# Performance work log

Measured on AMD Instinct MI355X. Metric: run time of the kernel, lower is better.

Reference implementation:

```python
import jax, jax.numpy as jnp
import numpy as np

B, F, S, D, H = 32, 4096, 8, 512, 2048
N_ITERS = 3
EPS = 1e-8
SCALE = D ** -0.5
LN_EPS = 1e-5  # torch LayerNorm default


def setup_inputs() -> dict:
    key = jax.random.key(0)
    ks = jax.random.split(key, 16)
    w = lambda k, shp: (jax.random.normal(k, shp) * 0.02).astype(jnp.float32)
    d = {
        "slots": jax.random.normal(ks[0], (B, S, D), dtype=jnp.float32),
        "features": jax.random.normal(ks[1], (B, F, D), dtype=jnp.float32),
        # projection weights, stored (in, out) so y = x @ W
        "w_k": w(ks[2], (D, D)),
        "w_v": w(ks[3], (D, D)),
        "w_q": w(ks[4], (D, D)),
        # layer norms
        "ln_feat_w": jnp.ones(D, jnp.float32), "ln_feat_b": jnp.zeros(D, jnp.float32),
        "ln_slot_w": jnp.ones(D, jnp.float32), "ln_slot_b": jnp.zeros(D, jnp.float32),
        # GRUCell (torch layout: gates [r, z, n] stacked on dim0 of [3D, D])
        "gru_w_ih": w(ks[5], (3 * D, D)),
        "gru_w_hh": w(ks[6], (3 * D, D)),
        "gru_b_ih": jnp.zeros(3 * D, jnp.float32),
        "gru_b_hh": jnp.zeros(3 * D, jnp.float32),
        # residual MLP: LN -> Linear(D,H) -> relu -> Linear(H,D)
        "ln_mlp_w": jnp.ones(D, jnp.float32), "ln_mlp_b": jnp.zeros(D, jnp.float32),
        "mlp_w1": w(ks[7], (D, H)), "mlp_b1": jnp.zeros(H, jnp.float32),
        "mlp_w2": w(ks[8], (H, D)), "mlp_b2": jnp.zeros(D, jnp.float32),
    }
    return d


def _ln(x, w, b):
    m = jnp.mean(x, axis=-1, keepdims=True)
    v = jnp.mean(jnp.square(x - m), axis=-1, keepdims=True)
    return (x - m) * jax.lax.rsqrt(v + LN_EPS) * w + b


def _gru_cell(x, h, w_ih, w_hh, b_ih, b_hh):
    # torch.nn.GRUCell semantics; x,h: [..., D]
    gi = x @ w_ih.T + b_ih
    gh = h @ w_hh.T + b_hh
    i_r, i_z, i_n = jnp.split(gi, 3, axis=-1)
    h_r, h_z, h_n = jnp.split(gh, 3, axis=-1)
    r = jax.nn.sigmoid(i_r + h_r)
    z = jax.nn.sigmoid(i_z + h_z)
    n = jnp.tanh(i_n + r * h_n)
    return (1.0 - z) * n + z * h


def reference(slots, features, w_k, w_v, w_q, ln_feat_w, ln_feat_b,
              ln_slot_w, ln_slot_b, gru_w_ih, gru_w_hh, gru_b_ih, gru_b_hh,
              ln_mlp_w, ln_mlp_b, mlp_w1, mlp_b1, mlp_w2, mlp_b2):
    f = _ln(features, ln_feat_w, ln_feat_b)          # [B,F,D]
    keys = f @ w_k                                    # [B,F,D]
    values = f @ w_v                                  # [B,F,D]
    pre_norm_attn = None
    for _ in range(N_ITERS):
        s_n = _ln(slots, ln_slot_w, ln_slot_b)        # [B,S,D]
        q = s_n @ w_q                                 # [B,S,D]
        dots = jnp.einsum('bsd,bfd->bsf', q, keys) * SCALE
        pre_norm_attn = jax.nn.softmax(dots, axis=1)  # softmax over SLOTS
        attn = pre_norm_attn + EPS
        attn = attn / jnp.sum(attn, axis=-1, keepdims=True)
        updates = jnp.einsum('bsf,bfd->bsd', attn, values)
        slots = _gru_cell(updates, s_n, gru_w_ih, gru_w_hh, gru_b_ih, gru_b_hh)
        # residual MLP with initial LayerNorm
        h = _ln(slots, ln_mlp_w, ln_mlp_b)
        h = jax.nn.relu(h @ mlp_w1 + mlp_b1) @ mlp_w2 + mlp_b2
        slots = slots + h
    return slots, pre_norm_attn
```

## Files before the change

kernel.cpp:

```cpp
#include <hip/hip_runtime.h>
#include <hip/hip_bf16.h>
#include <stdint.h>

typedef __hip_bfloat16 bf16;
typedef unsigned short ushort_t;

#define B_ 32
#define F_ 4096
#define S_ 8
#define D_ 512
#define H_ 2048
#define LN_EPS 1e-5f
#define EPS_ 1e-8f
#define SCALE_ 0.044194173824159216f

__device__ __forceinline__ float b2f(ushort_t u){
  union { uint32_t i; float f; } c; c.i = ((uint32_t)u) << 16; return c.f;
}
__device__ __forceinline__ float4 ld4f(const float* p){ return *(const float4*)p; }
__device__ __forceinline__ float4 ld4h(const ushort_t* p){
  ushort4 u = *(const ushort4*)p;
  return make_float4(b2f(u.x), b2f(u.y), b2f(u.z), b2f(u.w));
}
__device__ __forceinline__ float allsum64(float v){
  #pragma unroll
  for (int o = 1; o < 64; o <<= 1) v += __shfl_xor(v, o, 64);
  return v;
}
__device__ __forceinline__ float blockSum256(float v, float* sh){
  v = allsum64(v);
  int wid = threadIdx.x >> 6, lane = threadIdx.x & 63;
  __syncthreads();
  if (lane == 0) sh[wid] = v;
  __syncthreads();
  return sh[0] + sh[1] + sh[2] + sh[3];
}
__device__ __forceinline__ float dynld(const void* p, int i, bool f32){
  return f32 ? ((const float*)p)[i] : b2f(((const ushort_t*)p)[i]);
}

__global__ void detect_dtype(const uint32_t* __restrict__ w, int* __restrict__ flag){
  __shared__ int sh;
  if (threadIdx.x == 0) sh = 0;
  __syncthreads();
  int c = 0;
  for (int i = threadIdx.x; i < 4096; i += 256){
    uint32_t e = (w[i] >> 7) & 0xFF;
    if (e == 0 || e >= 0xBF) c++;
  }
  atomicAdd(&sh, c);
  __syncthreads();
  if (threadIdx.x == 0) *flag = (sh >= 100) ? 1 : 0;
}

template<int TRANS_B, int A_DYN, int B_DYN, int A_CMB>
__global__ __launch_bounds__(256) void gemm64(
    const void* __restrict__ A, const void* __restrict__ B,
    const void* __restrict__ Abias, float* __restrict__ C,
    int M, int N, int K, int kLen, size_t aPart, const int* __restrict__ flag)
{
  const bool f32 = (*flag != 0);
  const bool aF = A_DYN ? f32 : true;
  const bool bF = B_DYN ? f32 : true;
  __shared__ float As[16][68];
  __shared__ float Bs[16][68];
  const int tid = threadIdx.x;
  const int m0 = blockIdx.x * 64, n0 = blockIdx.y * 64;
  const int kBeg = blockIdx.z * kLen;
  const int tm = (tid & 15) * 4, tn = (tid >> 4) * 4;
  const int ar = tid >> 2;
  const int ac = (tid & 3) * 4;
  const int br = tid >> 4;
  const int bc = (tid & 15) * 4;
  float acc[4][4] = {};

  for (int kc = kBeg; kc < kBeg + kLen; kc += 16){
    size_t aidx = (size_t)(m0 + ar) * K + kc + ac;
    float4 a4;
    if (A_CMB){
      const float* Af = (const float*)A;
      float4 s0 = ld4f(Af + aidx);
      float4 s1 = ld4f(Af + aPart + aidx);
      float4 s2 = ld4f(Af + 2 * aPart + aidx);
      float4 s3 = ld4f(Af + 3 * aPart + aidx);
      float bx0 = dynld(Abias, kc + ac + 0, f32);
      float bx1 = dynld(Abias, kc + ac + 1, f32);
      float bx2 = dynld(Abias, kc + ac + 2, f32);
      float bx3 = dynld(Abias, kc + ac + 3, f32);
      a4.x = fmaxf(s0.x + s1.x + s2.x + s3.x + bx0, 0.0f);
      a4.y = fmaxf(s0.y + s1.y + s2.y + s3.y + bx1, 0.0f);
      a4.z = fmaxf(s0.z + s1.z + s2.z + s3.z + bx2, 0.0f);
      a4.w = fmaxf(s0.w + s1.w + s2.w + s3.w + bx3, 0.0f);
    } else {
      a4 = aF ? ld4f((const float*)A + aidx) : ld4h((const ushort_t*)A + aidx);
    }
    As[ac+0][ar] = a4.x; As[ac+1][ar] = a4.y; As[ac+2][ar] = a4.z; As[ac+3][ar] = a4.w;
    if (!TRANS_B){
      size_t bidx = (size_t)(kc + br) * N + n0 + bc;
      float4 b4 = bF ? ld4f((const float*)B + bidx) : ld4h((const ushort_t*)B + bidx);
      Bs[br][bc+0] = b4.x; Bs[br][bc+1] = b4.y; Bs[br][bc+2] = b4.z; Bs[br][bc+3] = b4.w;
    } else {
      size_t bidx = (size_t)(n0 + ar) * K + kc + ac;
      float4 b4 = bF ? ld4f((const float*)B + bidx) : ld4h((const ushort_t*)B + bidx);
      Bs[ac+0][ar] = b4.x; Bs[ac+1][ar] = b4.y; Bs[ac+2][ar] = b4.z; Bs[ac+3][ar] = b4.w;
    }
    __syncthreads();
    #pragma unroll
    for (int k = 0; k < 16; k++){
      float av[4], bv[4];
      #pragma unroll
      for (int i = 0; i < 4; i++) av[i] = As[k][tm + i];
      #pragma unroll
      for (int j = 0; j < 4; j++) bv[j] = Bs[k][tn + j];
      #pragma unroll
      for (int i = 0; i < 4; i++)
        #pragma unroll
        for (int j = 0; j < 4; j++) acc[i][j] += av[i] * bv[j];
    }
    __syncthreads();
  }
  #pragma unroll
  for (int i = 0; i < 4; i++)
    #pragma unroll
    for (int j = 0; j < 4; j++)
      C[((size_t)blockIdx.z * M + m0 + tm + i) * N + n0 + tn + j] = acc[i][j];
}

__global__ __launch_bounds__(256) void combine4(
    const float* __restrict__ in, float* __restrict__ out, int sz)
{
  int i = blockIdx.x * 256 + threadIdx.x;
  out[i] = in[i] + in[sz + i] + in[2 * sz + i] + in[3 * sz + i];
}

__global__ __launch_bounds__(256) void gemm_gigh(
    const float* __restrict__ Ud, const float* __restrict__ Wvih,
    const float* __restrict__ s_n, const void* __restrict__ w_hh,
    float* __restrict__ gip, float* __restrict__ ghp,
    const int* __restrict__ flag)
{
  const bool f32 = (*flag != 0);
  const bool doGh = blockIdx.z >= 4;
  const int kz = blockIdx.z & 3;
  __shared__ float As[16][68];
  __shared__ float Bs[16][68];
  const int tid = threadIdx.x;
  const int m0 = blockIdx.x * 64, n0 = blockIdx.y * 64;
  const int kBeg = kz * 128;
  const int tm = (tid & 15) * 4, tn = (tid >> 4) * 4;
  const int ar = tid >> 2;
  const int ac = (tid & 3) * 4;
  const int br = tid >> 4;
  const int bc = (tid & 15) * 4;
  const float* A = doGh ? s_n : Ud;
  float acc[4][4] = {};

  for (int kc = kBeg; kc < kBeg + 128; kc += 16){
    float4 a4 = ld4f(A + (size_t)(m0 + ar) * 512 + kc + ac);
    As[ac+0][ar] = a4.x; As[ac+1][ar] = a4.y; As[ac+2][ar] = a4.z; As[ac+3][ar] = a4.w;
    if (!doGh){
      float4 b4 = ld4f(Wvih + (size_t)(kc + br) * 1536 + n0 + bc);
      Bs[br][bc+0] = b4.x; Bs[br][bc+1] = b4.y; Bs[br][bc+2] = b4.z; Bs[br][bc+3] = b4.w;
    } else {
      size_t bidx = (size_t)(n0 + ar) * 512 + kc + ac;
      float4 b4 = f32 ? ld4f((const float*)w_hh + bidx)
                      : ld4h((const ushort_t*)w_hh + bidx);
      Bs[ac+0][ar] = b4.x; Bs[ac+1][ar] = b4.y; Bs[ac+2][ar] = b4.z; Bs[ac+3][ar] = b4.w;
    }
    __syncthreads();
    #pragma unroll
    for (int k = 0; k < 16; k++){
      float av[4], bv[4];
      #pragma unroll
      for (int i = 0; i < 4; i++) av[i] = As[k][tm + i];
      #pragma unroll
      for (int j = 0; j < 4; j++) bv[j] = Bs[k][tn + j];
      #pragma unroll
      for (int i = 0; i < 4; i++)
        #pragma unroll
        for (int j = 0; j < 4; j++) acc[i][j] += av[i] * bv[j];
    }
    __syncthreads();
  }
  float* C = (doGh ? ghp : gip) + (size_t)kz * 256 * 1536;
  #pragma unroll
  for (int i = 0; i < 4; i++)
    #pragma unroll
    for (int j = 0; j < 4; j++)
      C[(size_t)(m0 + tm + i) * 1536 + n0 + tn + j] = acc[i][j];
}

__global__ __launch_bounds__(256, 2) void big_pass(
    const void* __restrict__ features, const float* __restrict__ qkp,
    const void* __restrict__ lnw, const void* __restrict__ lnb,
    void* __restrict__ d_out_base, float* __restrict__ Upart,
    float* __restrict__ Rpart, const int* __restrict__ flag)
{
  const bool F32 = (*flag != 0);
  __shared__ float Ubuf[4][S_ * D_];
  __shared__ float Rbuf[4][S_];
  __shared__ float pbuf[S_][256];
  const int b = blockIdx.y;
  const int tid = threadIdx.x;
  const int wid = tid >> 6, lane = tid & 63;
  const int fblock = blockIdx.x * 256;
  const int f0 = fblock + wid * 64;

  float lw[8], lb[8];
  #pragma unroll
  for (int j = 0; j < 8; j++){
    int d = 8 * lane + j;
    lw[j] = dynld(lnw, d, F32);
    lb[j] = dynld(lnb, d, F32);
  }
  float qkr[8][8];
  #pragma unroll
  for (int s = 0; s < 8; s++){
    const float* qp = qkp + (size_t)(b * S_ + s) * D_ + 8 * lane;
    float4 q0 = ld4f(qp);
    float4 q1 = ld4f(qp + 4);
    #pragma unroll
    for (int p = 1; p < 4; p++){
      const float* qq = qp + (size_t)p * 131072;
      float4 t0 = ld4f(qq), t1 = ld4f(qq + 4);
      q0.x += t0.x; q0.y += t0.y; q0.z += t0.z; q0.w += t0.w;
      q1.x += t1.x; q1.y += t1.y; q1.z += t1.z; q1.w += t1.w;
    }
    qkr[s][0]=q0.x; qkr[s][1]=q0.y; qkr[s][2]=q0.z; qkr[s][3]=q0.w;
    qkr[s][4]=q1.x; qkr[s][5]=q1.y; qkr[s][6]=q1.z; qkr[s][7]=q1.w;
  }
  float U[8][8];
  #pragma unroll
  for (int s = 0; s < 8; s++)
    #pragma unroll
    for (int j = 0; j < 8; j++) U[s][j] = 0.0f;
  float racc[8] = {0,0,0,0,0,0,0,0};

  const size_t base = ((size_t)b * F_ + f0) * D_ + 8 * lane;
  const float* fbf = (const float*)features + base;
  const ushort_t* fbh = (const ushort_t*)features + base;
  float4 nf0 = {}, nf1 = {}; uint4 nh = {};
  if (F32){ nf0 = *(const float4*)fbf; nf1 = *(const float4*)(fbf + 4); }
  else    { nh  = *(const uint4*)fbh; }

  for (int r = 0; r < 64; r++){
    float x[8];
    if (F32){
      float4 c0 = nf0, c1 = nf1;
      if (r < 63){
        nf0 = *(const float4*)(fbf + (size_t)(r + 1) * D_);
        nf1 = *(const float4*)(fbf + (size_t)(r + 1) * D_ + 4);
      }
      x[0]=c0.x; x[1]=c0.y; x[2]=c0.z; x[3]=c0.w;
      x[4]=c1.x; x[5]=c1.y; x[6]=c1.z; x[7]=c1.w;
    } else {
      uint4 cx = nh;
      if (r < 63) nh = *(const uint4*)(fbh + (size_t)(r + 1) * D_);
      x[0]=b2f(cx.x & 0xffff); x[1]=b2f(cx.x >> 16);
      x[2]=b2f(cx.y & 0xffff); x[3]=b2f(cx.y >> 16);
      x[4]=b2f(cx.z & 0xffff); x[5]=b2f(cx.z >> 16);
      x[6]=b2f(cx.w & 0xffff); x[7]=b2f(cx.w >> 16);
    }
    float sum = 0.0f;
    #pragma unroll
    for (int j = 0; j < 8; j++) sum += x[j];
    float mean = allsum64(sum) * (1.0f / 512.0f);
    float var = 0.0f;
    #pragma unroll
    for (int j = 0; j < 8; j++){ x[j] -= mean; var += x[j] * x[j]; }
    var = allsum64(var) * (1.0f / 512.0f);
    float rstd = 1.0f / sqrtf(var + LN_EPS);
    float y[8];
    #pragma unroll
    for (int j = 0; j < 8; j++) y[j] = x[j] * rstd * lw[j] + lb[j];

    float dt[8];
    #pragma unroll
    for (int s = 0; s < 8; s++){
      float t = 0.0f;
      #pragma unroll
      for (int j = 0; j < 8; j++) t += qkr[s][j] * y[j];
      dt[s] = allsum64(t) * SCALE_;
    }
    float mx = dt[0];
    #pragma unroll
    for (int s = 1; s < 8; s++) mx = fmaxf(mx, dt[s]);
    float p[8]; float den = 0.0f;
    #pragma unroll
    for (int s = 0; s < 8; s++){ p[s] = __expf(dt[s] - mx); den += p[s]; }
    float inv = 1.0f / den;
    #pragma unroll
    for (int s = 0; s < 8; s++) p[s] *= inv;
    #pragma unroll
    for (int s = 0; s < 8; s++) if (lane == s) pbuf[s][wid * 64 + r] = p[s];
    #pragma unroll
    for (int s = 0; s < 8; s++){
      float pe = p[s] + EPS_;
      racc[s] += pe;
      #pragma unroll
      for (int j = 0; j < 8; j++) U[s][j] += pe * y[j];
    }
  }
  #pragma unroll
  for (int s = 0; s < 8; s++){
    float* ub = &Ubuf[wid][s * D_ + 8 * lane];
    *(float4*)ub     = make_float4(U[s][0], U[s][1], U[s][2], U[s][3]);
    *(float4*)(ub+4) = make_float4(U[s][4], U[s][5], U[s][6], U[s][7]);
  }
  #pragma unroll
  for (int s = 0; s < 8; s++) if (lane == s) Rbuf[wid][s] = racc[s];
  __syncthreads();
  float* up = Upart + (size_t)(b * 16 + blockIdx.x) * S_ * D_;
  for (int e = tid; e < S_ * D_; e += 256)
    up[e] = Ubuf[0][e] + Ubuf[1][e] + Ubuf[2][e] + Ubuf[3][e];
  if (tid < 8)
    Rpart[(b * 16 + blockIdx.x) * S_ + tid] =
        Rbuf[0][tid] + Rbuf[1][tid] + Rbuf[2][tid] + Rbuf[3][tid];
  #pragma unroll
  for (int s = 0; s < 8; s++){
    size_t oi = 131072 + ((size_t)(b * S_ + s)) * F_ + fblock + tid;
    float pv = pbuf[s][tid];
    if (F32) ((float*)d_out_base)[oi] = pv;
    else     ((bf16*)d_out_base)[oi] = __float2bfloat16(pv);
  }
}

__global__ __launch_bounds__(256) void reduce_updates(
    const float* __restrict__ Upart, const float* __restrict__ Rpart,
    float* __restrict__ Ud)
{
  __shared__ float rinv;
  int bs = blockIdx.x;
  int b = bs >> 3, s = bs & 7;
  int t = threadIdx.x;
  if (t == 0){
    float r = 0.0f;
    for (int w = 0; w < 16; w++) r += Rpart[(b * 16 + w) * S_ + s];
    rinv = 1.0f / r;
  }
  __syncthreads();
  const float* up = Upart + ((size_t)(b * 16) * S_ + s) * D_;
  float ri = rinv;
  #pragma unroll
  for (int u = 0; u < 2; u++){
    int e = t + u * 256;
    float acc = 0.0f;
    for (int w = 0; w < 16; w++) acc += up[(size_t)w * S_ * D_ + e];
    Ud[((size_t)(b * S_ + s)) * D_ + e] = acc * ri;
  }
}

__global__ __launch_bounds__(256) void ln_rows(
    const float* __restrict__ x, const void* __restrict__ w,
    const void* __restrict__ b, float* __restrict__ y, const int* __restrict__ flag)
{
  const bool f32 = (*flag != 0);
  __shared__ float sh[4];
  int row = blockIdx.x, t = threadIdx.x;
  const float* xr = x + (size_t)row * D_;
  float v0 = xr[t], v1 = xr[t + 256];
  float mean = blockSum256(v0 + v1, sh) * (1.0f / 512.0f);
  float d0 = v0 - mean, d1 = v1 - mean;
  float var = blockSum256(d0 * d0 + d1 * d1, sh) * (1.0f / 512.0f);
  float rstd = 1.0f / sqrtf(var + LN_EPS);
  float w0 = dynld(w, t, f32),       w1 = dynld(w, t + 256, f32);
  float b0 = dynld(b, t, f32),       b1 = dynld(b, t + 256, f32);
  y[(size_t)row * D_ + t]       = d0 * rstd * w0 + b0;
  y[(size_t)row * D_ + t + 256] = d1 * rstd * w1 + b1;
}

__global__ __launch_bounds__(256) void gru_combine(
    const float* __restrict__ gip, const float* __restrict__ ghp,
    const void* __restrict__ b_ih, const void* __restrict__ b_hh,
    const float* __restrict__ sn, const void* __restrict__ lw,
    const void* __restrict__ lb, float* __restrict__ snew,
    float* __restrict__ lnm, const int* __restrict__ flag)
{
  const bool f32 = (*flag != 0);
  __shared__ float sh[4];
  int row = blockIdx.x, t = threadIdx.x;
  const float* snr = sn + (size_t)row * D_;
  float v[2];
  #pragma unroll
  for (int u = 0; u < 2; u++){
    int d = t + u * 256;
    float ir = 0, iz = 0, in_ = 0, hr = 0, hz = 0, hn = 0;
    #pragma unroll
    for (int p = 0; p < 4; p++){
      const float* gp = gip + (size_t)p * 393216 + (size_t)row * 1536;
      const float* hp = ghp + (size_t)p * 393216 + (size_t)row * 1536;
      ir  += gp[d]; iz += gp[512 + d]; in_ += gp[1024 + d];
      hr  += hp[d]; hz += hp[512 + d]; hn  += hp[1024 + d];
    }
    ir  += dynld(b_ih, d, f32);
    iz  += dynld(b_ih, 512 + d, f32);
    in_ += dynld(b_ih, 1024 + d, f32);
    hr  += dynld(b_hh, d, f32);
    hz  += dynld(b_hh, 512 + d, f32);
    hn  += dynld(b_hh, 1024 + d, f32);
    float rg = 1.0f / (1.0f + __expf(-(ir + hr)));
    float zg = 1.0f / (1.0f + __expf(-(iz + hz)));
    float a  = in_ + rg * hn;
    float e2 = __expf(2.0f * a);
    float ng = 1.0f - 2.0f / (e2 + 1.0f);
    float h  = snr[d];
    v[u] = (1.0f - zg) * ng + zg * h;
    snew[(size_t)row * D_ + d] = v[u];
  }
  float mean = blockSum256(v[0] + v[1], sh) * (1.0f / 512.0f);
  float d0 = v[0] - mean, d1 = v[1] - mean;
  float var = blockSum256(d0 * d0 + d1 * d1, sh) * (1.0f / 512.0f);
  float rstd = 1.0f / sqrtf(var + LN_EPS);
  float w0 = dynld(lw, t, f32),       w1 = dynld(lw, t + 256, f32);
  float b0 = dynld(lb, t, f32),       b1 = dynld(lb, t + 256, f32);
  lnm[(size_t)row * D_ + t]       = d0 * rstd * w0 + b0;
  lnm[(size_t)row * D_ + t + 256] = d1 * rstd * w1 + b1;
}

template<int FINAL>
__global__ __launch_bounds__(256) void combine_h2(
    const float* __restrict__ snew, const float* __restrict__ h2p,
    const void* __restrict__ b2, float* __restrict__ slots,
    void* __restrict__ out, const int* __restrict__ flag)
{
  const bool f32 = (*flag != 0);
  int idx = blockIdx.x * 256 + threadIdx.x;
  int d = idx & 511;
  float bias = dynld(b2, d, f32);
  float v = snew[idx] + h2p[idx] + h2p[131072 + idx] + h2p[262144 + idx]
          + h2p[393216 + idx] + bias;
  slots[idx] = v;
  if (FINAL){
    if (f32) ((float*)out)[idx] = v;
    else     ((bf16*)out)[idx] = __float2bfloat16(v);
  }
}

__global__ __launch_bounds__(256) void cast_in(const void* __restrict__ in,
                                               float* __restrict__ out,
                                               const int* __restrict__ flag){
  const bool f32 = (*flag != 0);
  int i = blockIdx.x * 256 + threadIdx.x;
  out[i] = f32 ? ((const float*)in)[i] : b2f(((const ushort_t*)in)[i]);
}

extern "C" void kernel_launch(void* const* d_in, const int* in_sizes, int n_in,
                              void* d_out, int out_size, void* d_ws, size_t ws_size,
                              hipStream_t stream)
{
  const void* in_slots  = d_in[0];
  const void* features  = d_in[1];
  const void* w_k   = d_in[2];
  const void* w_v   = d_in[3];
  const void* w_q   = d_in[4];
  const void* ln_feat_w = d_in[5];
  const void* ln_feat_b = d_in[6];
  const void* ln_slot_w = d_in[7];
  const void* ln_slot_b = d_in[8];
  const void* w_ih  = d_in[9];
  const void* w_hh  = d_in[10];
  const void* b_ih  = d_in[11];
  const void* b_hh  = d_in[12];
  const void* ln_mlp_w = d_in[13];
  const void* ln_mlp_b = d_in[14];
  const void* mlp_w1 = d_in[15];
  const void* mlp_b1 = d_in[16];
  const void* mlp_w2 = d_in[17];
  const void* mlp_b2 = d_in[18];

  float* W     = (float*)d_ws;
  int*   flag  = (int*)d_ws;
  float* Wqk   = W + 64;
  float* slots = Wqk   + 262144;
  float* s_n   = slots + 131072;
  float* qkp   = s_n   + 131072;
  float* Ud    = qkp   + 524288;
  float* Rpart = Ud    + 131072;
  float* Upart = Rpart + 4096;
  float* gip   = Upart + 2097152;
  float* ghp   = gip   + 1572864;
  float* lnm   = ghp   + 1572864;
  float* snew  = lnm   + 131072;
  float* h1p   = snew  + 131072;
  float* h2p   = h1p   + 2097152;
  float* Wqkp  = h2p   + 524288;
  float* Wvih  = Wqkp  + 1048576;

  detect_dtype<<<1, 256, 0, stream>>>((const uint32_t*)features, flag);
  cast_in<<<512, 256, 0, stream>>>(in_slots, slots, flag);
  gemm64<1, 1, 1, 0><<<dim3(8, 8, 4), 256, 0, stream>>>(
      w_q, w_k, nullptr, Wqkp, 512, 512, 512, 128, 0, flag);
  combine4<<<1024, 256, 0, stream>>>(Wqkp, Wqk, 262144);
  gemm64<1, 1, 1, 0><<<dim3(8, 24, 1), 256, 0, stream>>>(
      w_v, w_ih, nullptr, Wvih, 512, 1536, 512, 512, 0, flag);

  for (int it = 0; it < 3; ++it){
    ln_rows<<<256, 256, 0, stream>>>(slots, ln_slot_w, ln_slot_b, s_n, flag);
    gemm64<0, 0, 0, 0><<<dim3(4, 8, 4), 256, 0, stream>>>(
        s_n, Wqk, nullptr, qkp, 256, 512, 512, 128, 0, flag);
    big_pass<<<dim3(16, 32), 256, 0, stream>>>(
        features, qkp, ln_feat_w, ln_feat_b, d_out, Upart, Rpart, flag);
    reduce_updates<<<256, 256, 0, stream>>>(Upart, Rpart, Ud);
    gemm_gigh<<<dim3(4, 24, 8), 256, 0, stream>>>(
        Ud, Wvih, s_n, w_hh, gip, ghp, flag);
    gru_combine<<<256, 256, 0, stream>>>(gip, ghp, b_ih, b_hh, s_n,
                                         ln_mlp_w, ln_mlp_b, snew, lnm, flag);
    gemm64<0, 0, 1, 0><<<dim3(4, 32, 4), 256, 0, stream>>>(
        lnm, mlp_w1, nullptr, h1p, 256, 2048, 512, 128, 0, flag);
    gemm64<0, 0, 1, 1><<<dim3(4, 8, 4), 256, 0, stream>>>(
        h1p, mlp_w2, mlp_b1, h2p, 256, 512, 2048, 512, 524288, flag);
    if (it < 2)
      combine_h2<0><<<512, 256, 0, stream>>>(snew, h2p, mlp_b2, slots, d_out, flag);
    else
      combine_h2<1><<<512, 256, 0, stream>>>(snew, h2p, mlp_b2, slots, d_out, flag);
  }
}
```

Before: 1.187 ms.

## Split big_pass into smaller blocks, template dtype path, fuse residual with slot LN

The feature pass now launches twice as many blocks, each covering 128 features instead of 256. Its shared-memory U buffer shrinks from 4x8x512 to 4x2x512 floats and is reduced in four staged rounds, which should raise occupancy. The row loop is templated on the dtype flag, which removes the runtime branch inside the loop. The final residual-add kernel now applies the next iteration's slot LayerNorm directly, removing a separate ln_rows launch per iteration. The second MLP GEMM uses an 8-way split-K. The costs are more partial sums for reduce_updates and combine to read and more barriers in the staged reduction.

Measured after the change: 1.052 ms. -11.4%, faster.

```diff
diff --git a/kernel.cpp b/kernel.cpp
--- a/kernel.cpp
+++ b/kernel.cpp
@@ -190,64 +190,23 @@
       C[(size_t)(m0 + tm + i) * 1536 + n0 + tn + j] = acc[i][j];
 }
 
-__global__ __launch_bounds__(256, 2) void big_pass(
-    const void* __restrict__ features, const float* __restrict__ qkp,
-    const void* __restrict__ lnw, const void* __restrict__ lnb,
-    void* __restrict__ d_out_base, float* __restrict__ Upart,
-    float* __restrict__ Rpart, const int* __restrict__ flag)
-{
-  const bool F32 = (*flag != 0);
-  __shared__ float Ubuf[4][S_ * D_];
-  __shared__ float Rbuf[4][S_];
-  __shared__ float pbuf[S_][256];
-  const int b = blockIdx.y;
-  const int tid = threadIdx.x;
-  const int wid = tid >> 6, lane = tid & 63;
-  const int fblock = blockIdx.x * 256;
-  const int f0 = fblock + wid * 64;
-
-  float lw[8], lb[8];
-  #pragma unroll
-  for (int j = 0; j < 8; j++){
-    int d = 8 * lane + j;
-    lw[j] = dynld(lnw, d, F32);
-    lb[j] = dynld(lnb, d, F32);
-  }
-  float qkr[8][8];
-  #pragma unroll
-  for (int s = 0; s < 8; s++){
-    const float* qp = qkp + (size_t)(b * S_ + s) * D_ + 8 * lane;
-    float4 q0 = ld4f(qp);
-    float4 q1 = ld4f(qp + 4);
-    #pragma unroll
-    for (int p = 1; p < 4; p++){
-      const float* qq = qp + (size_t)p * 131072;
-      float4 t0 = ld4f(qq), t1 = ld4f(qq + 4);
-      q0.x += t0.x; q0.y += t0.y; q0.z += t0.z; q0.w += t0.w;
-      q1.x += t1.x; q1.y += t1.y; q1.z += t1.z; q1.w += t1.w;
-    }
-    qkr[s][0]=q0.x; qkr[s][1]=q0.y; qkr[s][2]=q0.z; qkr[s][3]=q0.w;
-    qkr[s][4]=q1.x; qkr[s][5]=q1.y; qkr[s][6]=q1.z; qkr[s][7]=q1.w;
-  }
-  float U[8][8];
-  #pragma unroll
-  for (int s = 0; s < 8; s++)
-    #pragma unroll
-    for (int j = 0; j < 8; j++) U[s][j] = 0.0f;
-  float racc[8] = {0,0,0,0,0,0,0,0};
-
-  const size_t base = ((size_t)b * F_ + f0) * D_ + 8 * lane;
+template<int F32>
+__device__ __forceinline__ void bp_rows(
+    const void* __restrict__ features, size_t base,
+    const float (&lw)[8], const float (&lb)[8], const float (&qkr)[8][8],
+    float (&U)[8][8], float (&racc)[8], float (*pbuf)[128], int wid, int lane)
+{
   const float* fbf = (const float*)features + base;
   const ushort_t* fbh = (const ushort_t*)features + base;
   float4 nf0 = {}, nf1 = {}; uint4 nh = {};
   if (F32){ nf0 = *(const float4*)fbf; nf1 = *(const float4*)(fbf + 4); }
   else    { nh  = *(const uint4*)fbh; }
 
-  for (int r = 0; r < 64; r++){
+  for (int r = 0; r < 32; r++){
     float x[8];
     if (F32){
       float4 c0 = nf0, c1 = nf1;
-      if (r < 63){
+      if (r < 31){
         nf0 = *(const float4*)(fbf + (size_t)(r + 1) * D_);
         nf1 = *(const float4*)(fbf + (size_t)(r + 1) * D_ + 4);
       }
@@ -255,7 +214,7 @@
       x[4]=c1.x; x[5]=c1.y; x[6]=c1.z; x[7]=c1.w;
     } else {
       uint4 cx = nh;
-      if (r < 63) nh = *(const uint4*)(fbh + (size_t)(r + 1) * D_);
+      if (r < 31) nh = *(const uint4*)(fbh + (size_t)(r + 1) * D_);
       x[0]=b2f(cx.x & 0xffff); x[1]=b2f(cx.x >> 16);
       x[2]=b2f(cx.y & 0xffff); x[3]=b2f(cx.y >> 16);
       x[4]=b2f(cx.z & 0xffff); x[5]=b2f(cx.z >> 16);
@@ -292,7 +251,7 @@
     #pragma unroll
     for (int s = 0; s < 8; s++) p[s] *= inv;
     #pragma unroll
-    for (int s = 0; s < 8; s++) if (lane == s) pbuf[s][wid * 64 + r] = p[s];
+    for (int s = 0; s < 8; s++) if (lane == s) pbuf[s][wid * 32 + r] = p[s];
     #pragma unroll
     for (int s = 0; s < 8; s++){
       float pe = p[s] + EPS_;
@@ -301,27 +260,82 @@
       for (int j = 0; j < 8; j++) U[s][j] += pe * y[j];
     }
   }
+}
+
+__global__ __launch_bounds__(256, 2) void big_pass(
+    const void* __restrict__ features, const float* __restrict__ qkp,
+    const void* __restrict__ lnw, const void* __restrict__ lnb,
+    void* __restrict__ d_out_base, float* __restrict__ Upart,
+    float* __restrict__ Rpart, const int* __restrict__ flag)
+{
+  const bool f32rt = (*flag != 0);
+  __shared__ float Ubuf[4][2 * D_];
+  __shared__ float pbuf[S_][128];
+  __shared__ float Rbuf[4][S_];
+  const int b = blockIdx.y;
+  const int tid = threadIdx.x;
+  const int wid = tid >> 6, lane = tid & 63;
+  const int fblock = blockIdx.x * 128;
+  const int f0 = fblock + wid * 32;
+
+  float lw[8], lb[8];
+  #pragma unroll
+  for (int j = 0; j < 8; j++){
+    int d = 8 * lane + j;
+    lw[j] = dynld(lnw, d, f32rt);
+    lb[j] = dynld(lnb, d, f32rt);
+  }
+  float qkr[8][8];
   #pragma unroll
   for (int s = 0; s < 8; s++){
-    float* ub = &Ubuf[wid][s * D_ + 8 * lane];
-    *(float4*)ub     = make_float4(U[s][0], U[s][1], U[s][2], U[s][3]);
-    *(float4*)(ub+4) = make_float4(U[s][4], U[s][5], U[s][6], U[s][7]);
-  }
+    const float* qp = qkp + (size_t)(b * S_ + s) * D_ + 8 * lane;
+    float4 q0 = ld4f(qp);
+    float4 q1 = ld4f(qp + 4);
+    #pragma unroll
+    for (int p = 1; p < 4; p++){
+      const float* qq = qp + (size_t)p * 131072;
+      float4 t0 = ld4f(qq), t1 = ld4f(qq + 4);
+      q0.x += t0.x; q0.y += t0.y; q0.z += t0.z; q0.w += t0.w;
+      q1.x += t1.x; q1.y += t1.y; q1.z += t1.z; q1.w += t1.w;
+    }
+    qkr[s][0]=q0.x; qkr[s][1]=q0.y; qkr[s][2]=q0.z; qkr[s][3]=q0.w;
+    qkr[s][4]=q1.x; qkr[s][5]=q1.y; qkr[s][6]=q1.z; qkr[s][7]=q1.w;
+  }
+  float U[8][8] = {};
+  float racc[8] = {0,0,0,0,0,0,0,0};
+  const size_t base = ((size_t)b * F_ + f0) * D_ + 8 * lane;
+
+  if (f32rt) bp_rows<1>(features, base, lw, lb, qkr, U, racc, pbuf, wid, lane);
+  else       bp_rows<0>(features, base, lw, lb, qkr, U, racc, pbuf, wid, lane);
+
   #pragma unroll
   for (int s = 0; s < 8; s++) if (lane == s) Rbuf[wid][s] = racc[s];
   __syncthreads();
-  float* up = Upart + (size_t)(b * 16 + blockIdx.x) * S_ * D_;
-  for (int e = tid; e < S_ * D_; e += 256)
-    up[e] = Ubuf[0][e] + Ubuf[1][e] + Ubuf[2][e] + Ubuf[3][e];
+  #pragma unroll
+  for (int e2 = 0; e2 < 4; e2++){
+    int e = tid + e2 * 256;
+    int s = e >> 7, c = e & 127;
+    size_t oi = 131072 + ((size_t)(b * S_ + s)) * F_ + fblock + c;
+    float pv = pbuf[s][c];
+    if (f32rt) ((float*)d_out_base)[oi] = pv;
+    else       ((bf16*)d_out_base)[oi] = __float2bfloat16(pv);
+  }
   if (tid < 8)
-    Rpart[(b * 16 + blockIdx.x) * S_ + tid] =
+    Rpart[((size_t)b * 32 + blockIdx.x) * 8 + tid] =
         Rbuf[0][tid] + Rbuf[1][tid] + Rbuf[2][tid] + Rbuf[3][tid];
-  #pragma unroll
-  for (int s = 0; s < 8; s++){
-    size_t oi = 131072 + ((size_t)(b * S_ + s)) * F_ + fblock + tid;
-    float pv = pbuf[s][tid];
-    if (F32) ((float*)d_out_base)[oi] = pv;
-    else     ((bf16*)d_out_base)[oi] = __float2bfloat16(pv);
+  float* up = Upart + ((size_t)b * 32 + blockIdx.x) * (S_ * D_);
+  #pragma unroll
+  for (int g = 0; g < 4; g++){
+    #pragma unroll
+    for (int h = 0; h < 2; h++){
+      float* ub = &Ubuf[wid][h * D_ + 8 * lane];
+      *(float4*)ub     = make_float4(U[2*g+h][0], U[2*g+h][1], U[2*g+h][2], U[2*g+h][3]);
+      *(float4*)(ub+4) = make_float4(U[2*g+h][4], U[2*g+h][5], U[2*g+h][6], U[2*g+h][7]);
+    }
+    __syncthreads();
+    for (int e = tid; e < 2 * D_; e += 256)
+      up[g * 2 * D_ + e] = Ubuf[0][e] + Ubuf[1][e] + Ubuf[2][e] + Ubuf[3][e];
+    if (g < 3) __syncthreads();
   }
 }
 
@@ -335,17 +349,17 @@
   int t = threadIdx.x;
   if (t == 0){
     float r = 0.0f;
-    for (int w = 0; w < 16; w++) r += Rpart[(b * 16 + w) * S_ + s];
+    for (int w = 0; w < 32; w++) r += Rpart[((size_t)(b * 32 + w)) * 8 + s];
     rinv = 1.0f / r;
   }
   __syncthreads();
-  const float* up = Upart + ((size_t)(b * 16) * S_ + s) * D_;
+  const float* up = Upart + ((size_t)b * 32 * 8 + s) * 512;
   float ri = rinv;
   #pragma unroll
   for (int u = 0; u < 2; u++){
     int e = t + u * 256;
     float acc = 0.0f;
-    for (int w = 0; w < 16; w++) acc += up[(size_t)w * S_ * D_ + e];
+    for (int w = 0; w < 32; w++) acc += up[(size_t)w * 4096 + e];
     Ud[((size_t)(b * S_ + s)) * D_ + e] = acc * ri;
   }
 }
@@ -418,21 +432,39 @@
 }
 
 template<int FINAL>
-__global__ __launch_bounds__(256) void combine_h2(
+__global__ __launch_bounds__(256) void combine_ln(
     const float* __restrict__ snew, const float* __restrict__ h2p,
-    const void* __restrict__ b2, float* __restrict__ slots,
+    const void* __restrict__ b2, const void* __restrict__ lnw,
+    const void* __restrict__ lnb, float* __restrict__ s_n,
     void* __restrict__ out, const int* __restrict__ flag)
 {
   const bool f32 = (*flag != 0);
-  int idx = blockIdx.x * 256 + threadIdx.x;
-  int d = idx & 511;
-  float bias = dynld(b2, d, f32);
-  float v = snew[idx] + h2p[idx] + h2p[131072 + idx] + h2p[262144 + idx]
-          + h2p[393216 + idx] + bias;
-  slots[idx] = v;
-  if (FINAL){
-    if (f32) ((float*)out)[idx] = v;
-    else     ((bf16*)out)[idx] = __float2bfloat16(v);
+  __shared__ float sh[4];
+  int row = blockIdx.x, t = threadIdx.x;
+  float v[2];
+  #pragma unroll
+  for (int u = 0; u < 2; u++){
+    int d = t + u * 256;
+    size_t idx = (size_t)row * D_ + d;
+    float acc = snew[idx];
+    #pragma unroll
+    for (int p = 0; p < 8; p++) acc += h2p[(size_t)p * 131072 + idx];
+    acc += dynld(b2, d, f32);
+    v[u] = acc;
+    if (FINAL){
+      if (f32) ((float*)out)[idx] = acc;
+      else     ((bf16*)out)[idx] = __float2bfloat16(acc);
+    }
+  }
+  if (!FINAL){
+    float mean = blockSum256(v[0] + v[1], sh) * (1.0f / 512.0f);
+    float d0 = v[0] - mean, d1 = v[1] - mean;
+    float var = blockSum256(d0 * d0 + d1 * d1, sh) * (1.0f / 512.0f);
+    float rstd = 1.0f / sqrtf(var + LN_EPS);
+    float w0 = dynld(lnw, t, f32),       w1 = dynld(lnw, t + 256, f32);
+    float b0 = dynld(lnb, t, f32),       b1 = dynld(lnb, t + 256, f32);
+    s_n[(size_t)row * D_ + t]       = d0 * rstd * w0 + b0;
+    s_n[(size_t)row * D_ + t + 256] = d1 * rstd * w1 + b1;
   }
 }
 
@@ -476,14 +508,14 @@
   float* qkp   = s_n   + 131072;
   float* Ud    = qkp   + 524288;
   float* Rpart = Ud    + 131072;
-  float* Upart = Rpart + 4096;
-  float* gip   = Upart + 2097152;
+  float* Upart = Rpart + 8192;
+  float* gip   = Upart + 4194304;
   float* ghp   = gip   + 1572864;
   float* lnm   = ghp   + 1572864;
   float* snew  = lnm   + 131072;
   float* h1p   = snew  + 131072;
   float* h2p   = h1p   + 2097152;
-  float* Wqkp  = h2p   + 524288;
+  float* Wqkp  = h2p   + 1048576;
   float* Wvih  = Wqkp  + 1048576;
 
   detect_dtype<<<1, 256, 0, stream>>>((const uint32_t*)features, flag);
@@ -493,12 +525,12 @@
   combine4<<<1024, 256, 0, stream>>>(Wqkp, Wqk, 262144);
   gemm64<1, 1, 1, 0><<<dim3(8, 24, 1), 256, 0, stream>>>(
       w_v, w_ih, nullptr, Wvih, 512, 1536, 512, 512, 0, flag);
+  ln_rows<<<256, 256, 0, stream>>>(slots, ln_slot_w, ln_slot_b, s_n, flag);
 
   for (int it = 0; it < 3; ++it){
-    ln_rows<<<256, 256, 0, stream>>>(slots, ln_slot_w, ln_slot_b, s_n, flag);
     gemm64<0, 0, 0, 0><<<dim3(4, 8, 4), 256, 0, stream>>>(
         s_n, Wqk, nullptr, qkp, 256, 512, 512, 128, 0, flag);
-    big_pass<<<dim3(16, 32), 256, 0, stream>>>(
+    big_pass<<<dim3(32, 32), 256, 0, stream>>>(
         features, qkp, ln_feat_w, ln_feat_b, d_out, Upart, Rpart, flag);
     reduce_updates<<<256, 256, 0, stream>>>(Upart, Rpart, Ud);
     gemm_gigh<<<dim3(4, 24, 8), 256, 0, stream>>>(
@@ -507,11 +539,13 @@
                                          ln_mlp_w, ln_mlp_b, snew, lnm, flag);
     gemm64<0, 0, 1, 0><<<dim3(4, 32, 4), 256, 0, stream>>>(
         lnm, mlp_w1, nullptr, h1p, 256, 2048, 512, 128, 0, flag);
-    gemm64<0, 0, 1, 1><<<dim3(4, 8, 4), 256, 0, stream>>>(
-        h1p, mlp_w2, mlp_b1, h2p, 256, 512, 2048, 512, 524288, flag);
+    gemm64<0, 0, 1, 1><<<dim3(4, 8, 8), 256, 0, stream>>>(
+        h1p, mlp_w2, mlp_b1, h2p, 256, 512, 2048, 256, 524288, flag);
     if (it < 2)
-      combine_h2<0><<<512, 256, 0, stream>>>(snew, h2p, mlp_b2, slots, d_out, flag);
+      combine_ln<0><<<256, 256, 0, stream>>>(snew, h2p, mlp_b2, ln_slot_w,
+                                             ln_slot_b, s_n, d_out, flag);
     else
-      combine_h2<1><<<512, 256, 0, stream>>>(snew, h2p, mlp_b2, slots, d_out, flag);
-  }
-}
+      combine_ln<1><<<256, 256, 0, stream>>>(snew, h2p, mlp_b2, ln_slot_w,
+                                             ln_slot_b, s_n, d_out, flag);
+  }
+}
```
